# Kernel tuning notes

Measured on AMD Instinct MI355X. Metric: run time of the kernel, lower is better.

## Reference

```python
import jax, jax.numpy as jnp
import numpy as np

DIM = 2048
NUM_HEADS = 16
HEAD_DIM = DIM // NUM_HEADS
SCALE = 1.0 / np.sqrt(HEAD_DIM)


def setup_inputs() -> dict:
    key = jax.random.key(0)
    ks = jax.random.split(key, 5)
    B, S = 2, 2048
    w_std = 1.0 / np.sqrt(DIM)
    return {
        "hidden_states": jax.random.normal(ks[0], (B, S, DIM), dtype=jnp.float32),
        "Wq": jax.random.normal(ks[1], (DIM, DIM), dtype=jnp.float32) * w_std,
        "Wk": jax.random.normal(ks[2], (DIM, DIM), dtype=jnp.float32) * w_std,
        "Wv": jax.random.normal(ks[3], (DIM, DIM), dtype=jnp.float32) * w_std,
        "Wo": jax.random.normal(ks[4], (DIM, DIM), dtype=jnp.float32) * w_std,
    }


def reference(hidden_states, Wq, Wk, Wv, Wo):
    B, S, _ = hidden_states.shape
    # nn.Linear(dim, dim, bias=False): y = x @ W.T
    q = (hidden_states @ Wq.T).reshape(B, S, NUM_HEADS, HEAD_DIM)
    k = (hidden_states @ Wk.T).reshape(B, S, NUM_HEADS, HEAD_DIM)
    v = (hidden_states @ Wv.T).reshape(B, S, NUM_HEADS, HEAD_DIM)
    # Causal softmax attention (equivalent to the module's blockwise
    # online-softmax _efficient_attention, dropout = 0).
    scores = jnp.einsum("bqhd,bkhd->bhqk", q, k) * SCALE
    causal = jnp.tril(jnp.ones((S, S), dtype=bool))  # [S,S], True = keep
    scores = jnp.where(causal[None, None, :, :], scores, -jnp.inf)
    attn = jax.nn.softmax(scores, axis=-1)
    out = jnp.einsum("bhqk,bkhd->bqhd", attn, v).reshape(B, S, DIM)
    return out @ Wo.T
```

## Files before the change

kernel.cpp:

```cpp
#include <hip/hip_runtime.h>
#include <cmath>

typedef _Float16 f16x8 __attribute__((ext_vector_type(8)));
typedef _Float16 f16x4 __attribute__((ext_vector_type(4)));
typedef float    f32x4 __attribute__((ext_vector_type(4)));

#define LOG2E 1.4426950408889634f

__device__ __forceinline__ void load_lds16(const void* g, void* l) {
  __builtin_amdgcn_global_load_lds(
      (const __attribute__((address_space(1))) unsigned int*)g,
      (__attribute__((address_space(3))) unsigned int*)l, 16, 0, 0);
}

__global__ __launch_bounds__(256) void cvt_f32_f16(const float* __restrict__ in,
                                                   _Float16* __restrict__ out,
                                                   int n4) {
  int i = blockIdx.x * blockDim.x + threadIdx.x;
  int stride = gridDim.x * blockDim.x;
  for (; i < n4; i += stride) {
    float4 v = ((const float4*)in)[i];
    f16x4 h = { (_Float16)v.x, (_Float16)v.y, (_Float16)v.z, (_Float16)v.w };
    ((f16x4*)out)[i] = h;
  }
}

__device__ __forceinline__ void gemm_core(const _Float16* __restrict__ A,
                                          const _Float16* __restrict__ B,
                                          _Float16* Asm, _Float16* Bsm,
                                          f32x4 acc[4][4]) {
  const int tid  = threadIdx.x;
  const int wave = tid >> 6, lane = tid & 63;
  const int g = lane >> 4, l15 = lane & 15;
  const int wm = wave >> 1, wn = wave & 1;
  const int srow = tid >> 2, sslot = tid & 3;

  const _Float16* Abase = A + (size_t)(blockIdx.x * 128) * 2048;
  const _Float16* Bbase = B + (size_t)(blockIdx.y * 128) * 2048;

  for (int k0 = 0; k0 < 2048; k0 += 32) {
#pragma unroll
    for (int i = 0; i < 2; ++i) {
      int row = i * 64 + srow;
      int sp  = sslot ^ (row & 3);
      load_lds16(Abase + (size_t)row * 2048 + k0 + sp * 8,
                 (char*)Asm + i * 4096 + wave * 1024);
      load_lds16(Bbase + (size_t)row * 2048 + k0 + sp * 8,
                 (char*)Bsm + i * 4096 + wave * 1024);
    }
    __syncthreads();

    f16x8 af[4], bf[4];
#pragma unroll
    for (int mi = 0; mi < 4; ++mi) {
      int row = wm * 64 + mi * 16 + l15;
      af[mi] = *(const f16x8*)((const char*)Asm + row * 64 + ((g ^ (row & 3)) << 4));
    }
#pragma unroll
    for (int ni = 0; ni < 4; ++ni) {
      int row = wn * 64 + ni * 16 + l15;
      bf[ni] = *(const f16x8*)((const char*)Bsm + row * 64 + ((g ^ (row & 3)) << 4));
    }
#pragma unroll
    for (int mi = 0; mi < 4; ++mi)
#pragma unroll
      for (int ni = 0; ni < 4; ++ni)
        acc[mi][ni] = __builtin_amdgcn_mfma_f32_16x16x32_f16(af[mi], bf[ni],
                                                             acc[mi][ni], 0, 0, 0);
    __syncthreads();
  }
}

__global__ __launch_bounds__(256) void gemm_qkv(
    const _Float16* __restrict__ Xh,
    const _Float16* __restrict__ Wq, const _Float16* __restrict__ Wk,
    const _Float16* __restrict__ Wv,
    _Float16* __restrict__ Qb, _Float16* __restrict__ Kb,
    _Float16* __restrict__ Vt, float qscale) {
  __shared__ _Float16 Asm[128 * 32], Bsm[128 * 32];
  const int z = blockIdx.z;
  const _Float16* B = (z == 0) ? Wq : (z == 1) ? Wk : Wv;
  f32x4 acc[4][4] = {};
  gemm_core(Xh, B, Asm, Bsm, acc);

  const int tid = threadIdx.x;
  const int wave = tid >> 6, lane = tid & 63;
  const int g = lane >> 4, l15 = lane & 15;
  const int wm = wave >> 1, wn = wave & 1;
  const float scale = (z == 0) ? qscale : 1.0f;
#pragma unroll
  for (int mi = 0; mi < 4; ++mi)
#pragma unroll
    for (int ni = 0; ni < 4; ++ni)
#pragma unroll
      for (int r = 0; r < 4; ++r) {
        int row = blockIdx.x * 128 + wm * 64 + mi * 16 + g * 4 + r;
        int col = blockIdx.y * 128 + wn * 64 + ni * 16 + l15;
        float v = acc[mi][ni][r] * scale;
        int b = row >> 11, sq = row & 2047, h = col >> 7, d = col & 127;
        if (z < 2) {
          _Float16* dst = (z == 0) ? Qb : Kb;
          dst[(((size_t)b * 16 + h) * 2048 + sq) * 128 + d] = (_Float16)v;
        } else {
          Vt[(((size_t)b * 16 + h) * 128 + d) * 2048 + sq] = (_Float16)v;
        }
      }
}

__global__ __launch_bounds__(256) void gemm_out(
    const _Float16* __restrict__ AO, const _Float16* __restrict__ Wo,
    float* __restrict__ C) {
  __shared__ _Float16 Asm[128 * 32], Bsm[128 * 32];
  f32x4 acc[4][4] = {};
  gemm_core(AO, Wo, Asm, Bsm, acc);

  const int tid = threadIdx.x;
  const int wave = tid >> 6, lane = tid & 63;
  const int g = lane >> 4, l15 = lane & 15;
  const int wm = wave >> 1, wn = wave & 1;
#pragma unroll
  for (int mi = 0; mi < 4; ++mi)
#pragma unroll
    for (int ni = 0; ni < 4; ++ni)
#pragma unroll
      for (int r = 0; r < 4; ++r) {
        int row = blockIdx.x * 128 + wm * 64 + mi * 16 + g * 4 + r;
        int col = blockIdx.y * 128 + wn * 64 + ni * 16 + l15;
        C[(size_t)row * 2048 + col] = acc[mi][ni][r];
      }
}

__global__ __launch_bounds__(256) void attn_fwd(
    const _Float16* __restrict__ Qb, const _Float16* __restrict__ Kb,
    const _Float16* __restrict__ Vt, _Float16* __restrict__ AO) {
  const int qt = blockIdx.x, bh = blockIdx.y;
  const int tid = threadIdx.x;
  const int wave = tid >> 6, lane = tid & 63;
  const int g = lane >> 4, l15 = lane & 15;

  __shared__ _Float16 Ksm[64 * 128];
  __shared__ _Float16 Vsm[128 * 64];
  __shared__ char     Psm[4][2048];

  const _Float16* qp = Qb + ((size_t)bh * 2048 + qt * 64 + wave * 16 + l15) * 128;
  f16x8 qf[4];
#pragma unroll
  for (int c = 0; c < 4; ++c) qf[c] = *(const f16x8*)(qp + c * 32 + g * 8);

  f32x4 po[8] = {};
  float m[4], lsum[4];
#pragma unroll
  for (int r = 0; r < 4; ++r) { m[r] = -1e30f; lsum[r] = 0.f; }

  char* P = &Psm[wave][0];

  for (int t = 0; t <= qt; ++t) {
#pragma unroll
    for (int i = 0; i < 4; ++i) {
      int krow = i * 16 + (tid >> 4);
      int ksp  = (tid & 15) ^ (krow & 15);
      load_lds16(Kb + ((size_t)bh * 2048 + t * 64 + krow) * 128 + ksp * 8,
                 (char*)Ksm + i * 4096 + wave * 1024);
      int vrow = i * 32 + (tid >> 3);
      int vsp  = (tid & 7) ^ (vrow & 7);
      load_lds16(Vt + ((size_t)bh * 128 + vrow) * 2048 + t * 64 + vsp * 8,
                 (char*)Vsm + i * 4096 + wave * 1024);
    }
    __syncthreads();

    f32x4 s[4];
#pragma unroll
    for (int n = 0; n < 4; ++n) {
      f32x4 a = {0.f, 0.f, 0.f, 0.f};
#pragma unroll
      for (int c = 0; c < 4; ++c) {
        int krow = n * 16 + l15;
        int sp   = (c * 4 + g) ^ (krow & 15);
        f16x8 kf = *(const f16x8*)((const char*)Ksm + krow * 256 + (sp << 4));
        a = __builtin_amdgcn_mfma_f32_16x16x32_f16(qf[c], kf, a, 0, 0, 0);
      }
      s[n] = a;
    }

    if (t == qt) {
#pragma unroll
      for (int n = 0; n < 4; ++n)
#pragma unroll
        for (int r = 0; r < 4; ++r) {
          int key = n * 16 + l15;
          int qr  = wave * 16 + g * 4 + r;
          if (key > qr) s[n][r] = -1e30f;
        }
    }

#pragma unroll
    for (int r = 0; r < 4; ++r) {
      float mx = fmaxf(fmaxf(s[0][r], s[1][r]), fmaxf(s[2][r], s[3][r]));
#pragma unroll
      for (int off = 1; off < 16; off <<= 1) mx = fmaxf(mx, __shfl_xor(mx, off));
      float mn = fmaxf(m[r], mx);
      float sc = exp2f(m[r] - mn);
      m[r] = mn;
      float rs = 0.f;
#pragma unroll
      for (int n = 0; n < 4; ++n) {
        float p = exp2f(s[n][r] - mn);
        s[n][r] = p;
        rs += p;
      }
#pragma unroll
      for (int off = 1; off < 16; off <<= 1) rs += __shfl_xor(rs, off);
      lsum[r] = lsum[r] * sc + rs;
#pragma unroll
      for (int no = 0; no < 8; ++no) po[no][r] *= sc;
    }

#pragma unroll
    for (int n = 0; n < 4; ++n)
#pragma unroll
      for (int r = 0; r < 4; ++r) {
        int row = g * 4 + r, key = n * 16 + l15;
        int slot = key >> 3;
        *(_Float16*)(P + row * 128 + ((slot ^ (row & 7)) << 4) + (key & 7) * 2) =
            (_Float16)s[n][r];
      }

    f16x8 pf[2];
#pragma unroll
    for (int kc = 0; kc < 2; ++kc) {
      int sp = (kc * 4 + g) ^ (l15 & 7);
      pf[kc] = *(const f16x8*)(P + l15 * 128 + (sp << 4));
    }
#pragma unroll
    for (int no = 0; no < 8; ++no)
#pragma unroll
      for (int kc = 0; kc < 2; ++kc) {
        int vrow = no * 16 + l15;
        int sp   = (kc * 4 + g) ^ (vrow & 7);
        f16x8 vf = *(const f16x8*)((const char*)Vsm + vrow * 128 + (sp << 4));
        po[no] = __builtin_amdgcn_mfma_f32_16x16x32_f16(pf[kc], vf, po[no], 0, 0, 0);
      }

    __syncthreads();
  }

  const int b = bh >> 4, h = bh & 15;
#pragma unroll
  for (int no = 0; no < 8; ++no)
#pragma unroll
    for (int r = 0; r < 4; ++r) {
      float v = po[no][r] / lsum[r];
      size_t row = (size_t)b * 2048 + qt * 64 + wave * 16 + g * 4 + r;
      int col = h * 128 + no * 16 + l15;
      AO[row * 2048 + col] = (_Float16)v;
    }
}

extern "C" void kernel_launch(void* const* d_in, const int* in_sizes, int n_in,
                              void* d_out, int out_size, void* d_ws, size_t ws_size,
                              hipStream_t stream) {
  const float* X  = (const float*)d_in[0];
  const float* Wq = (const float*)d_in[1];
  const float* Wk = (const float*)d_in[2];
  const float* Wv = (const float*)d_in[3];
  const float* Wo = (const float*)d_in[4];
  float* out = (float*)d_out;

  char* ws = (char*)d_ws;
  _Float16* Xh  = (_Float16*)(ws);
  _Float16* Wqh = (_Float16*)(ws + (16u << 20));
  _Float16* Wkh = (_Float16*)(ws + (24u << 20));
  _Float16* Wvh = (_Float16*)(ws + (32u << 20));
  _Float16* Woh = (_Float16*)(ws + (40u << 20));
  _Float16* Qb  = (_Float16*)(ws + (48u << 20));
  _Float16* Kb  = (_Float16*)(ws + (64u << 20));
  _Float16* Vt  = (_Float16*)(ws + (80u << 20));
  _Float16* AO  = (_Float16*)(ws + (96u << 20));

  cvt_f32_f16<<<2048, 256, 0, stream>>>(X,  Xh,  8388608 / 4);
  cvt_f32_f16<<<1024, 256, 0, stream>>>(Wq, Wqh, 4194304 / 4);
  cvt_f32_f16<<<1024, 256, 0, stream>>>(Wk, Wkh, 4194304 / 4);
  cvt_f32_f16<<<1024, 256, 0, stream>>>(Wv, Wvh, 4194304 / 4);
  cvt_f32_f16<<<1024, 256, 0, stream>>>(Wo, Woh, 4194304 / 4);

  const float qscale = LOG2E / sqrtf(128.0f);
  gemm_qkv<<<dim3(32, 16, 3), 256, 0, stream>>>(Xh, Wqh, Wkh, Wvh, Qb, Kb, Vt, qscale);
  attn_fwd<<<dim3(32, 32), 256, 0, stream>>>(Qb, Kb, Vt, AO);
  gemm_out<<<dim3(32, 16), 256, 0, stream>>>(AO, Woh, out);
}
```

Baseline: 502.9 us.

## Enlarge attention query tile, double-buffer K/V, reorder blocks, batch weight casts

The attention kernel now gives each block 128 query rows, with 32 rows per wave, so every K/V tile loaded into LDS serves twice as many queries. K/V tiles are double-buffered so the next tile loads while the current one is computed. A flat grid maps blocks to XCDs by head and launches the longest causal rows first, and the final division becomes a reciprocal multiply. The four weight conversions are merged into one launch. The cost is more registers and LDS per block, plus idle waves on the diagonal tile.

New measurement: 449.9 us. 1.12x faster.

```diff
diff --git a/kernel.cpp b/kernel.cpp
--- a/kernel.cpp
+++ b/kernel.cpp
@@ -16,6 +16,28 @@
 __global__ __launch_bounds__(256) void cvt_f32_f16(const float* __restrict__ in,
                                                    _Float16* __restrict__ out,
                                                    int n4) {
+  int i = blockIdx.x * blockDim.x + threadIdx.x;
+  int stride = gridDim.x * blockDim.x;
+  for (; i < n4; i += stride) {
+    float4 v = ((const float4*)in)[i];
+    f16x4 h = { (_Float16)v.x, (_Float16)v.y, (_Float16)v.z, (_Float16)v.w };
+    ((f16x4*)out)[i] = h;
+  }
+}
+
+__global__ __launch_bounds__(256) void cvt_w4(const float* __restrict__ w0,
+                                              const float* __restrict__ w1,
+                                              const float* __restrict__ w2,
+                                              const float* __restrict__ w3,
+                                              _Float16* __restrict__ o0,
+                                              _Float16* __restrict__ o1,
+                                              _Float16* __restrict__ o2,
+                                              _Float16* __restrict__ o3,
+                                              int n4) {
+  const float* in = (blockIdx.y == 0) ? w0 : (blockIdx.y == 1) ? w1
+                  : (blockIdx.y == 2) ? w2 : w3;
+  _Float16* out = (blockIdx.y == 0) ? o0 : (blockIdx.y == 1) ? o1
+                : (blockIdx.y == 2) ? o2 : o3;
   int i = blockIdx.x * blockDim.x + threadIdx.x;
   int stride = gridDim.x * blockDim.x;
   for (; i < n4; i += stride) {
@@ -130,129 +152,172 @@
       }
 }
 
-__global__ __launch_bounds__(256) void attn_fwd(
+__global__ __launch_bounds__(256, 2) void attn_fwd(
     const _Float16* __restrict__ Qb, const _Float16* __restrict__ Kb,
     const _Float16* __restrict__ Vt, _Float16* __restrict__ AO) {
-  const int qt = blockIdx.x, bh = blockIdx.y;
+  const int id  = blockIdx.x;
+  const int xcd = id & 7, j = id >> 3;
+  const int bh  = xcd * 4 + (j & 3);
+  const int qb  = 15 - (j >> 2);
+
   const int tid = threadIdx.x;
   const int wave = tid >> 6, lane = tid & 63;
   const int g = lane >> 4, l15 = lane & 15;
 
-  __shared__ _Float16 Ksm[64 * 128];
-  __shared__ _Float16 Vsm[128 * 64];
-  __shared__ char     Psm[4][2048];
-
-  const _Float16* qp = Qb + ((size_t)bh * 2048 + qt * 64 + wave * 16 + l15) * 128;
-  f16x8 qf[4];
-#pragma unroll
-  for (int c = 0; c < 4; ++c) qf[c] = *(const f16x8*)(qp + c * 32 + g * 8);
-
-  f32x4 po[8] = {};
-  float m[4], lsum[4];
-#pragma unroll
-  for (int r = 0; r < 4; ++r) { m[r] = -1e30f; lsum[r] = 0.f; }
-
-  char* P = &Psm[wave][0];
-
-  for (int t = 0; t <= qt; ++t) {
+  __shared__ _Float16 Ksm[2][64 * 128];
+  __shared__ _Float16 Vsm[2][64 * 128];
+  __shared__ _Float16 Psm[4][32 * 64];
+
+  const _Float16* qp =
+      Qb + ((size_t)bh * 2048 + qb * 128 + wave * 32 + l15) * 128;
+  f16x8 qf[2][4];
+#pragma unroll
+  for (int mi = 0; mi < 2; ++mi)
+#pragma unroll
+    for (int c = 0; c < 4; ++c)
+      qf[mi][c] = *(const f16x8*)(qp + mi * 16 * 128 + c * 32 + g * 8);
+
+  f32x4 po[2][8] = {};
+  float m[2][4], lsum[2][4];
+#pragma unroll
+  for (int mi = 0; mi < 2; ++mi)
+#pragma unroll
+    for (int r = 0; r < 4; ++r) { m[mi][r] = -1e30f; lsum[mi][r] = 0.f; }
+
+  char* Pb = (char*)&Psm[wave][0];
+  const int NT  = 2 * qb + 2;
+  const int NTw = 2 * qb + 1 + (wave >> 1);
+  const int dt  = 2 * qb + (wave >> 1);
+
+  const int k_i  = tid >> 4, k_sp = (tid & 15) ^ (tid >> 4);
+  const int v_i  = tid >> 3, v_sp = (tid & 7) ^ ((tid >> 3) & 7);
+  const _Float16* kbase = Kb + (size_t)bh * 2048 * 128;
+  const _Float16* vbase = Vt + (size_t)bh * 128 * 2048;
+
+  auto stage = [&](int buf, int t) {
+    char* kdst = (char*)&Ksm[buf][0] + wave * 1024;
+    char* vdst = (char*)&Vsm[buf][0] + wave * 1024;
+    const _Float16* kb = kbase + (size_t)t * 64 * 128;
+    const _Float16* vb = vbase + t * 64;
 #pragma unroll
     for (int i = 0; i < 4; ++i) {
-      int krow = i * 16 + (tid >> 4);
-      int ksp  = (tid & 15) ^ (krow & 15);
-      load_lds16(Kb + ((size_t)bh * 2048 + t * 64 + krow) * 128 + ksp * 8,
-                 (char*)Ksm + i * 4096 + wave * 1024);
-      int vrow = i * 32 + (tid >> 3);
-      int vsp  = (tid & 7) ^ (vrow & 7);
-      load_lds16(Vt + ((size_t)bh * 128 + vrow) * 2048 + t * 64 + vsp * 8,
-                 (char*)Vsm + i * 4096 + wave * 1024);
-    }
+      load_lds16(kb + (size_t)(i * 16 + k_i) * 128 + k_sp * 8, kdst + i * 4096);
+      load_lds16(vb + (size_t)(i * 32 + v_i) * 2048 + v_sp * 8, vdst + i * 4096);
+    }
+  };
+
+  stage(0, 0);
+  __syncthreads();
+
+  int buf = 0;
+  for (int t = 0; t < NT; ++t) {
+    if (t + 1 < NT) stage(buf ^ 1, t + 1);
+
+    if (t < NTw) {
+      const char* Kl = (const char*)&Ksm[buf][0];
+      const char* Vl = (const char*)&Vsm[buf][0];
+
+      f32x4 s[2][4];
+#pragma unroll
+      for (int n = 0; n < 4; ++n) {
+        f32x4 a0 = {0.f, 0.f, 0.f, 0.f}, a1 = {0.f, 0.f, 0.f, 0.f};
+#pragma unroll
+        for (int c = 0; c < 4; ++c) {
+          int slot = (c * 4 + g) ^ l15;
+          f16x8 kf = *(const f16x8*)(Kl + (n * 16 + l15) * 256 + (slot << 4));
+          a0 = __builtin_amdgcn_mfma_f32_16x16x32_f16(qf[0][c], kf, a0, 0, 0, 0);
+          a1 = __builtin_amdgcn_mfma_f32_16x16x32_f16(qf[1][c], kf, a1, 0, 0, 0);
+        }
+        s[0][n] = a0; s[1][n] = a1;
+      }
+
+      if (t == dt) {
+#pragma unroll
+        for (int mi = 0; mi < 2; ++mi)
+#pragma unroll
+          for (int n = 0; n < 4; ++n)
+#pragma unroll
+            for (int r = 0; r < 4; ++r) {
+              int key = t * 64 + n * 16 + l15;
+              int qr  = qb * 128 + wave * 32 + mi * 16 + g * 4 + r;
+              if (key > qr) s[mi][n][r] = -1e30f;
+            }
+      }
+
+#pragma unroll
+      for (int mi = 0; mi < 2; ++mi)
+#pragma unroll
+        for (int r = 0; r < 4; ++r) {
+          float mx = fmaxf(fmaxf(s[mi][0][r], s[mi][1][r]),
+                           fmaxf(s[mi][2][r], s[mi][3][r]));
+#pragma unroll
+          for (int off = 1; off < 16; off <<= 1) mx = fmaxf(mx, __shfl_xor(mx, off));
+          float mn = fmaxf(m[mi][r], mx);
+          float sc = exp2f(m[mi][r] - mn);
+          m[mi][r] = mn;
+          float rs = 0.f;
+#pragma unroll
+          for (int n = 0; n < 4; ++n) {
+            float p = exp2f(s[mi][n][r] - mn);
+            s[mi][n][r] = p;
+            rs += p;
+          }
+#pragma unroll
+          for (int off = 1; off < 16; off <<= 1) rs += __shfl_xor(rs, off);
+          lsum[mi][r] = lsum[mi][r] * sc + rs;
+#pragma unroll
+          for (int no = 0; no < 8; ++no) po[mi][no][r] *= sc;
+        }
+
+#pragma unroll
+      for (int mi = 0; mi < 2; ++mi)
+#pragma unroll
+        for (int n = 0; n < 4; ++n)
+#pragma unroll
+          for (int r = 0; r < 4; ++r) {
+            int row = mi * 16 + g * 4 + r, key = n * 16 + l15;
+            *(_Float16*)(Pb + row * 128 + (((key >> 3) ^ (row & 7)) << 4) +
+                         (key & 7) * 2) = (_Float16)s[mi][n][r];
+          }
+
+      f16x8 pf[2][2];
+#pragma unroll
+      for (int mi = 0; mi < 2; ++mi)
+#pragma unroll
+        for (int kc = 0; kc < 2; ++kc) {
+          int slot = (kc * 4 + g) ^ (l15 & 7);
+          pf[mi][kc] = *(const f16x8*)(Pb + (mi * 16 + l15) * 128 + (slot << 4));
+        }
+#pragma unroll
+      for (int no = 0; no < 8; ++no)
+#pragma unroll
+        for (int kc = 0; kc < 2; ++kc) {
+          int vrow = no * 16 + l15;
+          int slot = (kc * 4 + g) ^ (l15 & 7);
+          f16x8 vf = *(const f16x8*)(Vl + vrow * 128 + (slot << 4));
+          po[0][no] = __builtin_amdgcn_mfma_f32_16x16x32_f16(pf[0][kc], vf,
+                                                             po[0][no], 0, 0, 0);
+          po[1][no] = __builtin_amdgcn_mfma_f32_16x16x32_f16(pf[1][kc], vf,
+                                                             po[1][no], 0, 0, 0);
+        }
+    }
+
     __syncthreads();
-
-    f32x4 s[4];
-#pragma unroll
-    for (int n = 0; n < 4; ++n) {
-      f32x4 a = {0.f, 0.f, 0.f, 0.f};
-#pragma unroll
-      for (int c = 0; c < 4; ++c) {
-        int krow = n * 16 + l15;
-        int sp   = (c * 4 + g) ^ (krow & 15);
-        f16x8 kf = *(const f16x8*)((const char*)Ksm + krow * 256 + (sp << 4));
-        a = __builtin_amdgcn_mfma_f32_16x16x32_f16(qf[c], kf, a, 0, 0, 0);
-      }
-      s[n] = a;
-    }
-
-    if (t == qt) {
-#pragma unroll
-      for (int n = 0; n < 4; ++n)
-#pragma unroll
-        for (int r = 0; r < 4; ++r) {
-          int key = n * 16 + l15;
-          int qr  = wave * 16 + g * 4 + r;
-          if (key > qr) s[n][r] = -1e30f;
-        }
-    }
-
+    buf ^= 1;
+  }
+
+  const int b = bh >> 4, h = bh & 15;
+#pragma unroll
+  for (int mi = 0; mi < 2; ++mi)
 #pragma unroll
     for (int r = 0; r < 4; ++r) {
-      float mx = fmaxf(fmaxf(s[0][r], s[1][r]), fmaxf(s[2][r], s[3][r]));
-#pragma unroll
-      for (int off = 1; off < 16; off <<= 1) mx = fmaxf(mx, __shfl_xor(mx, off));
-      float mn = fmaxf(m[r], mx);
-      float sc = exp2f(m[r] - mn);
-      m[r] = mn;
-      float rs = 0.f;
-#pragma unroll
-      for (int n = 0; n < 4; ++n) {
-        float p = exp2f(s[n][r] - mn);
-        s[n][r] = p;
-        rs += p;
-      }
-#pragma unroll
-      for (int off = 1; off < 16; off <<= 1) rs += __shfl_xor(rs, off);
-      lsum[r] = lsum[r] * sc + rs;
-#pragma unroll
-      for (int no = 0; no < 8; ++no) po[no][r] *= sc;
-    }
-
-#pragma unroll
-    for (int n = 0; n < 4; ++n)
-#pragma unroll
-      for (int r = 0; r < 4; ++r) {
-        int row = g * 4 + r, key = n * 16 + l15;
-        int slot = key >> 3;
-        *(_Float16*)(P + row * 128 + ((slot ^ (row & 7)) << 4) + (key & 7) * 2) =
-            (_Float16)s[n][r];
-      }
-
-    f16x8 pf[2];
-#pragma unroll
-    for (int kc = 0; kc < 2; ++kc) {
-      int sp = (kc * 4 + g) ^ (l15 & 7);
-      pf[kc] = *(const f16x8*)(P + l15 * 128 + (sp << 4));
-    }
-#pragma unroll
-    for (int no = 0; no < 8; ++no)
-#pragma unroll
-      for (int kc = 0; kc < 2; ++kc) {
-        int vrow = no * 16 + l15;
-        int sp   = (kc * 4 + g) ^ (vrow & 7);
-        f16x8 vf = *(const f16x8*)((const char*)Vsm + vrow * 128 + (sp << 4));
-        po[no] = __builtin_amdgcn_mfma_f32_16x16x32_f16(pf[kc], vf, po[no], 0, 0, 0);
-      }
-
-    __syncthreads();
-  }
-
-  const int b = bh >> 4, h = bh & 15;
-#pragma unroll
-  for (int no = 0; no < 8; ++no)
-#pragma unroll
-    for (int r = 0; r < 4; ++r) {
-      float v = po[no][r] / lsum[r];
-      size_t row = (size_t)b * 2048 + qt * 64 + wave * 16 + g * 4 + r;
-      int col = h * 128 + no * 16 + l15;
-      AO[row * 2048 + col] = (_Float16)v;
+      float inv = 1.0f / lsum[mi][r];
+      size_t row = (size_t)b * 2048 + qb * 128 + wave * 32 + mi * 16 + g * 4 + r;
+#pragma unroll
+      for (int no = 0; no < 8; ++no) {
+        int col = h * 128 + no * 16 + l15;
+        AO[row * 2048 + col] = (_Float16)(po[mi][no][r] * inv);
+      }
     }
 }
 
@@ -277,14 +342,12 @@
   _Float16* Vt  = (_Float16*)(ws + (80u << 20));
   _Float16* AO  = (_Float16*)(ws + (96u << 20));
 
-  cvt_f32_f16<<<2048, 256, 0, stream>>>(X,  Xh,  8388608 / 4);
-  cvt_f32_f16<<<1024, 256, 0, stream>>>(Wq, Wqh, 4194304 / 4);
-  cvt_f32_f16<<<1024, 256, 0, stream>>>(Wk, Wkh, 4194304 / 4);
-  cvt_f32_f16<<<1024, 256, 0, stream>>>(Wv, Wvh, 4194304 / 4);
-  cvt_f32_f16<<<1024, 256, 0, stream>>>(Wo, Woh, 4194304 / 4);
+  cvt_f32_f16<<<2048, 256, 0, stream>>>(X, Xh, 8388608 / 4);
+  cvt_w4<<<dim3(512, 4), 256, 0, stream>>>(Wq, Wk, Wv, Wo, Wqh, Wkh, Wvh, Woh,
+                                           4194304 / 4);
 
   const float qscale = LOG2E / sqrtf(128.0f);
   gemm_qkv<<<dim3(32, 16, 3), 256, 0, stream>>>(Xh, Wqh, Wkh, Wvh, Qb, Kb, Vt, qscale);
-  attn_fwd<<<dim3(32, 32), 256, 0, stream>>>(Qb, Kb, Vt, AO);
+  attn_fwd<<<512, 256, 0, stream>>>(Qb, Kb, Vt, AO);
   gemm_out<<<dim3(32, 16), 256, 0, stream>>>(AO, Woh, out);
 }
```
